# Kernel tuning notes

Hardware: AMD Instinct MI355X
Metric: run time of the kernel (lower is better)

Reference implementation:

```python
import jax, jax.numpy as jnp
import numpy as np

VOCAB = 50000
BATCH = 1024
SEQ = 120
NFEAT = 1
EMBED = 50
HIDDEN = 300
NCLASS = 5
FORGET_BIAS = 1.0  # tf.nn.rnn_cell.LSTMCell default


def setup_inputs() -> dict:
    key = jax.random.key(0)
    k1, k2, k3, k4 = jax.random.split(key, 4)
    input_ids = jax.random.randint(k1, (BATCH, SEQ, NFEAT), 0, VOCAB)
    embeddings = jax.random.normal(k2, (VOCAB, EMBED), jnp.float32)
    # LSTM kernel acts on concat([x, h]) -> 4*H gates (i, j, f, o order, TF convention)
    in_dim = NFEAT * EMBED + HIDDEN
    W_lstm = jax.random.normal(k3, (in_dim, 4 * HIDDEN), jnp.float32) * (1.0 / np.sqrt(in_dim))
    b_lstm = jnp.zeros((4 * HIDDEN,), jnp.float32)
    U = jax.random.normal(k4, (HIDDEN, NCLASS), jnp.float32) * (1.0 / np.sqrt(HIDDEN))
    b2 = jnp.zeros((NCLASS,), jnp.float32)
    return {"input_ids": input_ids, "embeddings": embeddings,
            "W_lstm": W_lstm, "b_lstm": b_lstm, "U": U, "b2": b2}


def reference(input_ids, embeddings, W_lstm, b_lstm, U, b2):
    B, T, F = input_ids.shape
    # embedding lookup + flatten feature dim: (B, T, F*E)
    x = embeddings[input_ids].reshape(B, T, -1)
    H = b_lstm.shape[0] // 4

    def cell(carry, x_t):
        c, h = carry
        z = jnp.concatenate([x_t, h], axis=-1) @ W_lstm + b_lstm  # (B, 4H)
        i, j, f, o = jnp.split(z, 4, axis=-1)  # TF LSTMCell gate order
        c_new = c * jax.nn.sigmoid(f + FORGET_BIAS) + jax.nn.sigmoid(i) * jnp.tanh(j)
        h_new = jnp.tanh(c_new) * jax.nn.sigmoid(o)
        return (c_new, h_new), h_new

    c0 = jnp.zeros((B, H), x.dtype)
    h0 = jnp.zeros((B, H), x.dtype)
    # scan over time; outputs are (T, B, H) which matches the module's final
    # transpose([1,0,2]) of the (B, T, C) preds.
    _, outs = jax.lax.scan(cell, (c0, h0), jnp.swapaxes(x, 0, 1))
    # dropout placeholder is 1.0 at inference -> identity
    preds = outs @ U + b2  # (T, B, n_classes)
    return preds
```

## Files before the change

kernel.cpp:

```cpp
#include <hip/hip_runtime.h>
#include <hip/hip_bf16.h>


#define NB 1024
#define NT 120
#define NE 50
#define NH 300
#define KX 64
#define KH 320
#define KT 384
#define HP 320
#define NGRP 8
#define NCOLB 19
#define ROLES 20
#define GRID 160
#define WCOL_STRIDE 784
#define HSLOTS 8

typedef __bf16 bf16_t;
typedef __bf16 bf16x8 __attribute__((ext_vector_type(8)));
typedef float f32x4 __attribute__((ext_vector_type(4)));

__device__ __forceinline__ float fsig(float x) {
    return __builtin_amdgcn_rcpf(1.0f + __expf(-x));
}
__device__ __forceinline__ float ftanh(float x) {
    return fmaf(2.0f, __builtin_amdgcn_rcpf(1.0f + __expf(-2.0f * x)), -1.0f);
}

__device__ __forceinline__ bf16x8 coh_load8(const bf16_t* p) {
    const unsigned long long* q = (const unsigned long long*)p;
    union { unsigned long long u[2]; bf16x8 v; } t;
    t.u[0] = __hip_atomic_load(q,     __ATOMIC_RELAXED, __HIP_MEMORY_SCOPE_AGENT);
    t.u[1] = __hip_atomic_load(q + 1, __ATOMIC_RELAXED, __HIP_MEMORY_SCOPE_AGENT);
    return t.v;
}
__device__ __forceinline__ void coh_store16(bf16_t* p, bf16_t h) {
    __hip_atomic_store((unsigned short*)p, __builtin_bit_cast(unsigned short, h),
                       __ATOMIC_RELAXED, __HIP_MEMORY_SCOPE_AGENT);
}
__device__ __forceinline__ unsigned coh_loadu(const unsigned* p) {
    return __hip_atomic_load(p, __ATOMIC_RELAXED, __HIP_MEMORY_SCOPE_AGENT);
}
__device__ __forceinline__ void cnt_bump(unsigned* p) {
    __hip_atomic_fetch_add(p, 1u, __ATOMIC_RELAXED, __HIP_MEMORY_SCOPE_AGENT);
}

__device__ __forceinline__ void inv_l1() {
    asm volatile("buffer_inv sc0\n\ts_waitcnt vmcnt(0)" ::: "memory");
}
__device__ __forceinline__ unsigned xcc_id() {
    unsigned x;
    asm volatile("s_getreg_b32 %0, hwreg(HW_REG_XCC_ID)" : "=s"(x));
    return x & 0xfu;
}

__global__ void prep_all(const int* __restrict__ ids, const float* __restrict__ emb,
                         const float* __restrict__ W,
                         bf16_t* __restrict__ WpT, uint4* __restrict__ zbase,
                         int nzero, bf16_t* __restrict__ Xp) {
    const long stride = (long)gridDim.x * 256;
    const long g0 = (long)blockIdx.x * 256 + threadIdx.x;

    for (long i = g0; i < nzero; i += stride)
        zbase[i] = make_uint4(0u, 0u, 0u, 0u);

    for (long gid = g0; gid < 4 * HP * KT; gid += stride) {
        int k = (int)(gid % KT);
        int col = (int)(gid / KT);
        int g = col / HP, hc = col % HP;
        int kp = -1;
        if (k < 50) kp = k;
        else if (k >= 64 && k < 364) kp = k - 14;
        float v = 0.0f;
        if (kp >= 0 && hc < NH) v = W[(long)kp * 1200 + g * NH + hc];
        WpT[gid] = (bf16_t)v;
    }

    for (long gid = g0; gid < (long)NB * NT * 4; gid += stride) {
        int s = (int)(gid & 3);
        long bt = gid >> 2;
        int b = (int)(bt / NT), t = (int)(bt % NT);
        int id = ids[bt];
        const float* er = emb + (long)id * NE;
        bf16_t* dst = Xp + ((long)t * NB + b) * KX + s * 16;
#pragma unroll
        for (int j = 0; j < 16; ++j) {
            int e = s * 16 + j;
            dst[j] = (bf16_t)((e < NE) ? er[e] : 0.0f);
        }
    }
}

__global__ void __launch_bounds__(512, 2) lstm_persist(
    const float* __restrict__ bl, const bf16_t* __restrict__ WpT,
    bf16_t* Hbase,
    const bf16_t* __restrict__ Xp,
    unsigned* gcnt, unsigned* pcnt, unsigned* xcdA,
    const float* __restrict__ U, const float* __restrict__ b2,
    float* __restrict__ out)
{
    __shared__ __align__(16) unsigned char smem[64 * WCOL_STRIDE];
    __shared__ int sLocalOK;
    const int blk = blockIdx.x;
    const int tid = threadIdx.x;
    const int g = blk & 7;
    const int c = blk >> 3;
    const int lane = tid & 63, wave = tid >> 6;

    if (tid == 0)
        __hip_atomic_store(xcdA + blk, xcc_id() + 1u,
                           __ATOMIC_RELAXED, __HIP_MEMORY_SCOPE_AGENT);
    if (wave == 0) {
        unsigned v = 1u;
        for (;;) {
            if (lane < ROLES)
                v = coh_loadu(xcdA + (lane * NGRP + g));
            if (__all(v != 0)) break;
            __builtin_amdgcn_s_sleep(1);
        }
        unsigned ref = __shfl(v, 0, 64);
        int ok = __all(lane >= ROLES || v == ref);
        if (lane == 0) sLocalOK = ok;
    }

    unsigned* gC = gcnt + (long)g * NT;
    unsigned* pC = pcnt + (long)g * NT;
    const size_t HSZ = (size_t)NB * KH;

    if (c < NCOLB) {
        for (int ch = tid; ch < 64 * 48; ch += 512) {
            int col = ch / 48, pq = ch % 48;
            int gt = col >> 4, mm = col & 15;
            int hc = c * 16 + mm;
            const uint4* src = (const uint4*)(WpT + (long)(gt * HP + hc) * KT) + pq;
            *(uint4*)(smem + col * WCOL_STRIDE + pq * 16) = *src;
        }

        const int m = lane & 15, quad = lane >> 4;
        const int rbase = g * 128 + wave * 16;
        const int rowA  = rbase + m;
        const int hcOut = c * 16 + m;
        const bool colOK = (hcOut < NH);

        float bias[4] = {0.f, 0.f, 0.f, 0.f};
        if (colOK) {
#pragma unroll
            for (int gt = 0; gt < 4; ++gt) bias[gt] = bl[gt * NH + hcOut];
        }
        float cst[4] = {0.f, 0.f, 0.f, 0.f};

        __syncthreads();
        const bool localOK = (sLocalOK != 0);

        bf16x8 Bh[8][4];
#pragma unroll
        for (int kk = 0; kk < 8; ++kk)
#pragma unroll
            for (int gt = 0; gt < 4; ++gt) {
                Bh[kk][gt] = *(const bf16x8*)(smem + (gt * 16 + m) * WCOL_STRIDE
                                              + ((kk + 2) * 4 + quad) * 16);
                asm volatile("" : "+v"(Bh[kk][gt]));
            }

        for (int t = 0; t < NT; ++t) {
            const bf16x8* xv = (const bf16x8*)(Xp + ((long)t * NB + rowA) * KX);
            bf16x8 ax[2];
#pragma unroll
            for (int kk = 0; kk < 2; ++kk) ax[kk] = xv[kk * 4 + quad];

            f32x4 acc[4];
#pragma unroll
            for (int gt = 0; gt < 4; ++gt)
                acc[gt] = (f32x4){bias[gt], bias[gt], bias[gt], bias[gt]};
#pragma unroll
            for (int kk = 0; kk < 2; ++kk) {
#pragma unroll
                for (int gt = 0; gt < 4; ++gt) {
                    bf16x8 b = *(const bf16x8*)(smem + (gt * 16 + m) * WCOL_STRIDE
                                                + (kk * 4 + quad) * 16);
                    acc[gt] = __builtin_amdgcn_mfma_f32_16x16x32_bf16(ax[kk], b, acc[gt], 0, 0, 0);
                }
            }

            if (t > 0) {
                if (wave == 0) {
                    unsigned* gcp = gC + (t - 1);
                    unsigned* pcp = pC + (t - HSLOTS);
                    const bool needP = (t >= HSLOTS);
                    for (;;) {
                        unsigned v = 19u;
                        if (lane == 0)               v = coh_loadu(gcp);
                        else if (lane == 1 && needP) v = 18u + coh_loadu(pcp);
                        if (__all(v >= 19u)) break;
                        __builtin_amdgcn_s_sleep(1);
                    }
                    if (localOK) inv_l1();
                }
            }
            __syncthreads();
            __builtin_amdgcn_sched_barrier(0);

            const bf16_t* Hr = Hbase + (size_t)((t + HSLOTS - 1) & (HSLOTS - 1)) * HSZ;
            bf16_t*       Hw = Hbase + (size_t)(t & (HSLOTS - 1)) * HSZ;

            const bf16_t* hp = Hr + (long)rowA * KH;
            bf16x8 ah[10];
            if (localOK) {
                const bf16x8* hv = (const bf16x8*)hp;
#pragma unroll
                for (int i = 0; i < 10; ++i) ah[i] = hv[i * 4 + quad];
            } else {
#pragma unroll
                for (int i = 0; i < 10; ++i) ah[i] = coh_load8(hp + (i * 4 + quad) * 8);
            }
            __builtin_amdgcn_sched_barrier(0);

#pragma unroll
            for (int kk = 2; kk < 10; ++kk) {
#pragma unroll
                for (int gt = 0; gt < 4; ++gt)
                    acc[gt] = __builtin_amdgcn_mfma_f32_16x16x32_bf16(
                        ah[kk - 2], Bh[kk - 2][gt], acc[gt], 0, 0, 0);
            }
#pragma unroll
            for (int kk = 10; kk < 12; ++kk) {
#pragma unroll
                for (int gt = 0; gt < 4; ++gt) {
                    bf16x8 b = *(const bf16x8*)(smem + (gt * 16 + m) * WCOL_STRIDE
                                                + (kk * 4 + quad) * 16);
                    acc[gt] = __builtin_amdgcn_mfma_f32_16x16x32_bf16(ah[kk - 2], b, acc[gt], 0, 0, 0);
                }
            }

#pragma unroll
            for (int r = 0; r < 4; ++r) {
                float zi = acc[0][r];
                float zj = acc[1][r];
                float zf = acc[2][r];
                float zo = acc[3][r];
                float cn = cst[r] * fsig(zf + 1.0f) + fsig(zi) * ftanh(zj);
                cst[r] = cn;
                float hn = ftanh(cn) * fsig(zo);
                if (colOK) {
                    bf16_t* dst = Hw + (long)(rbase + quad * 4 + r) * KH + hcOut;
                    if (localOK) *dst = (bf16_t)hn;
                    else coh_store16(dst, (bf16_t)hn);
                }
            }

            __syncthreads();
            if (tid == 0) cnt_bump(gC + t);
        }
    } else {
        bf16_t* UThi = (bf16_t*)smem;
        bf16_t* UTlo = (bf16_t*)(smem + 10240);
        for (int i = tid; i < 16 * 320; i += 512) {
            int n = i / 320, k = i % 320;
            float v = (n < 5 && k < NH) ? U[k * 5 + n] : 0.0f;
            bf16_t hi = (bf16_t)v;
            UThi[i] = hi;
            UTlo[i] = (bf16_t)(v - (float)hi);
        }
        const int m = lane & 15, quad = lane >> 4;
        const float b2v = (m < 5) ? b2[m] : 0.0f;
        __syncthreads();
        const bool localOK = (sLocalOK != 0);

        bf16x8 Bu[10][2];
#pragma unroll
        for (int kk = 0; kk < 10; ++kk) {
            Bu[kk][0] = *(const bf16x8*)(UThi + m * 320 + kk * 32 + quad * 8);
            asm volatile("" : "+v"(Bu[kk][0]));
            Bu[kk][1] = *(const bf16x8*)(UTlo + m * 320 + kk * 32 + quad * 8);
            asm volatile("" : "+v"(Bu[kk][1]));
        }
        const int row0 = g * 128 + wave * 16 + m;

        for (int t = 0; t < NT; ++t) {
            if (wave == 0) {
                unsigned* gcp = gC + t;
                for (;;) {
                    unsigned v = 19u;
                    if (lane == 0) v = coh_loadu(gcp);
                    if (__all(v >= 19u)) break;
                    __builtin_amdgcn_s_sleep(1);
                }
                if (localOK) inv_l1();
            }
            __syncthreads();
            __builtin_amdgcn_sched_barrier(0);

            const bf16_t* Hs = Hbase + (size_t)(t & (HSLOTS - 1)) * HSZ;
            const bf16_t* hp = Hs + (long)row0 * KH;
            bf16x8 ah[10];
            if (localOK) {
                const bf16x8* hv = (const bf16x8*)hp;
#pragma unroll
                for (int i = 0; i < 10; ++i) ah[i] = hv[i * 4 + quad];
            } else {
#pragma unroll
                for (int i = 0; i < 10; ++i) ah[i] = coh_load8(hp + (i * 4 + quad) * 8);
            }
            __builtin_amdgcn_sched_barrier(0);

            f32x4 acc = (f32x4){0.f, 0.f, 0.f, 0.f};
#pragma unroll
            for (int kk = 0; kk < 10; ++kk) {
                acc = __builtin_amdgcn_mfma_f32_16x16x32_bf16(ah[kk], Bu[kk][0], acc, 0, 0, 0);
                acc = __builtin_amdgcn_mfma_f32_16x16x32_bf16(ah[kk], Bu[kk][1], acc, 0, 0, 0);
            }

            if (m < 5) {
#pragma unroll
                for (int r = 0; r < 4; ++r) {
                    int row = g * 128 + wave * 16 + quad * 4 + r;
                    out[(long)t * (NB * 5) + row * 5 + m] = acc[r] + b2v;
                }
            }

            __syncthreads();
            if (tid == 0) cnt_bump(pC + t);
        }
    }
}

extern "C" void kernel_launch(void* const* d_in, const int* in_sizes, int n_in,
                              void* d_out, int out_size, void* d_ws, size_t ws_size,
                              hipStream_t stream) {
    const int* ids   = (const int*)d_in[0];
    const float* emb = (const float*)d_in[1];
    const float* W   = (const float*)d_in[2];
    const float* bl  = (const float*)d_in[3];
    const float* U   = (const float*)d_in[4];
    const float* b2  = (const float*)d_in[5];
    float* out = (float*)d_out;

    char* ws = (char*)d_ws;
    bf16_t*   WpT   = (bf16_t*)ws;
    bf16_t*   Hbase = (bf16_t*)(ws + 983040);
    unsigned* gcnt  = (unsigned*)(ws + 6225920);
    unsigned* pcnt  = (unsigned*)(ws + 6229760);
    unsigned* xcdA  = (unsigned*)(ws + 6233600);
    bf16_t*   Xp    = (bf16_t*)(ws + 6234240);

    prep_all<<<2048, 256, 0, stream>>>(ids, emb, W, WpT,
                                       (uint4*)(ws + 983040), 328200, Xp);

    void* kargs[] = { (void*)&bl, (void*)&WpT, (void*)&Hbase, (void*)&Xp,
                      (void*)&gcnt, (void*)&pcnt, (void*)&xcdA,
                      (void*)&U, (void*)&b2, (void*)&out };
    hipError_t err = hipLaunchCooperativeKernel((const void*)lstm_persist,
                                                dim3(GRID), dim3(512), kargs, 0, stream);
    if (err != hipSuccess) {
        lstm_persist<<<GRID, 512, 0, stream>>>(bl, WpT, Hbase, Xp,
                                               gcnt, pcnt, xcdA, U, b2, out);
    }
}
```

Baseline: 641.5 us.

## Halve waves per block and keep all LSTM weights in registers

Each block now runs 4 waves instead of 8, and each wave handles two 16-row tiles. Every weight fragment, including the input and tail K-slices, now sits in registers loaded straight from global memory, so the LDS staging and the per-step LDS weight reads are gone. The aim is to cut LDS traffic and synchronisation per step and to reuse each weight fragment across two row tiles. The cost is much higher register pressure per wave and fewer waves to hide the latency of the h loads and the MFMA chain.

```diff
diff --git a/kernel.cpp b/kernel.cpp
--- a/kernel.cpp
+++ b/kernel.cpp
@@ -14,7 +14,6 @@
 #define NCOLB 19
 #define ROLES 20
 #define GRID 160
-#define WCOL_STRIDE 784
 #define HSLOTS 8
 
 typedef __bf16 bf16_t;
@@ -92,7 +91,7 @@
     }
 }
 
-__global__ void __launch_bounds__(512, 2) lstm_persist(
+__global__ void __launch_bounds__(256, 1) lstm_persist(
     const float* __restrict__ bl, const bf16_t* __restrict__ WpT,
     bf16_t* Hbase,
     const bf16_t* __restrict__ Xp,
@@ -100,7 +99,7 @@
     const float* __restrict__ U, const float* __restrict__ b2,
     float* __restrict__ out)
 {
-    __shared__ __align__(16) unsigned char smem[64 * WCOL_STRIDE];
+    __shared__ __align__(16) unsigned char smem[20608];
     __shared__ int sLocalOK;
     const int blk = blockIdx.x;
     const int tid = threadIdx.x;
@@ -127,19 +126,12 @@
     unsigned* gC = gcnt + (long)g * NT;
     unsigned* pC = pcnt + (long)g * NT;
     const size_t HSZ = (size_t)NB * KH;
+    const int m = lane & 15, quad = lane >> 4;
 
     if (c < NCOLB) {
-        for (int ch = tid; ch < 64 * 48; ch += 512) {
-            int col = ch / 48, pq = ch % 48;
-            int gt = col >> 4, mm = col & 15;
-            int hc = c * 16 + mm;
-            const uint4* src = (const uint4*)(WpT + (long)(gt * HP + hc) * KT) + pq;
-            *(uint4*)(smem + col * WCOL_STRIDE + pq * 16) = *src;
-        }
-
-        const int m = lane & 15, quad = lane >> 4;
-        const int rbase = g * 128 + wave * 16;
-        const int rowA  = rbase + m;
+        const int rbase = g * 128 + wave * 32;
+        const int rowA0 = rbase + m;
+        const int rowA1 = rbase + 16 + m;
         const int hcOut = c * 16 + m;
         const bool colOK = (hcOut < NH);
 
@@ -148,38 +140,43 @@
 #pragma unroll
             for (int gt = 0; gt < 4; ++gt) bias[gt] = bl[gt * NH + hcOut];
         }
-        float cst[4] = {0.f, 0.f, 0.f, 0.f};
+        float cst[2][4] = {};
+
+        bf16x8 B[12][4];
+#pragma unroll
+        for (int kk = 0; kk < 12; ++kk)
+#pragma unroll
+            for (int gt = 0; gt < 4; ++gt) {
+                B[kk][gt] = *(const bf16x8*)(WpT + ((long)(gt * HP + hcOut) * KT)
+                                             + kk * 32 + quad * 8);
+                asm volatile("" : "+v"(B[kk][gt]));
+            }
 
         __syncthreads();
         const bool localOK = (sLocalOK != 0);
 
-        bf16x8 Bh[8][4];
-#pragma unroll
-        for (int kk = 0; kk < 8; ++kk)
-#pragma unroll
-            for (int gt = 0; gt < 4; ++gt) {
-                Bh[kk][gt] = *(const bf16x8*)(smem + (gt * 16 + m) * WCOL_STRIDE
-                                              + ((kk + 2) * 4 + quad) * 16);
-                asm volatile("" : "+v"(Bh[kk][gt]));
-            }
-
         for (int t = 0; t < NT; ++t) {
-            const bf16x8* xv = (const bf16x8*)(Xp + ((long)t * NB + rowA) * KX);
-            bf16x8 ax[2];
-#pragma unroll
-            for (int kk = 0; kk < 2; ++kk) ax[kk] = xv[kk * 4 + quad];
-
-            f32x4 acc[4];
-#pragma unroll
-            for (int gt = 0; gt < 4; ++gt)
-                acc[gt] = (f32x4){bias[gt], bias[gt], bias[gt], bias[gt]};
+            const bf16x8* xv0 = (const bf16x8*)(Xp + ((long)t * NB + rowA0) * KX);
+            const bf16x8* xv1 = (const bf16x8*)(Xp + ((long)t * NB + rowA1) * KX);
+            bf16x8 ax0[2], ax1[2];
 #pragma unroll
             for (int kk = 0; kk < 2; ++kk) {
+                ax0[kk] = xv0[kk * 4 + quad];
+                ax1[kk] = xv1[kk * 4 + quad];
+            }
+
+            f32x4 acc[2][4];
+#pragma unroll
+            for (int rt = 0; rt < 2; ++rt)
+#pragma unroll
+                for (int gt = 0; gt < 4; ++gt)
+                    acc[rt][gt] = (f32x4){bias[gt], bias[gt], bias[gt], bias[gt]};
+#pragma unroll
+            for (int kk = 0; kk < 2; ++kk) {
 #pragma unroll
                 for (int gt = 0; gt < 4; ++gt) {
-                    bf16x8 b = *(const bf16x8*)(smem + (gt * 16 + m) * WCOL_STRIDE
-                                                + (kk * 4 + quad) * 16);
-                    acc[gt] = __builtin_amdgcn_mfma_f32_16x16x32_bf16(ax[kk], b, acc[gt], 0, 0, 0);
+                    acc[0][gt] = __builtin_amdgcn_mfma_f32_16x16x32_bf16(ax0[kk], B[kk][gt], acc[0][gt], 0, 0, 0);
+                    acc[1][gt] = __builtin_amdgcn_mfma_f32_16x16x32_bf16(ax1[kk], B[kk][gt], acc[1][gt], 0, 0, 0);
                 }
             }
 
@@ -204,48 +201,51 @@
             const bf16_t* Hr = Hbase + (size_t)((t + HSLOTS - 1) & (HSLOTS - 1)) * HSZ;
             bf16_t*       Hw = Hbase + (size_t)(t & (HSLOTS - 1)) * HSZ;
 
-            const bf16_t* hp = Hr + (long)rowA * KH;
-            bf16x8 ah[10];
+            const bf16_t* h0p = Hr + (long)rowA0 * KH;
+            const bf16_t* h1p = Hr + (long)rowA1 * KH;
+            bf16x8 ah0[10], ah1[10];
             if (localOK) {
-                const bf16x8* hv = (const bf16x8*)hp;
-#pragma unroll
-                for (int i = 0; i < 10; ++i) ah[i] = hv[i * 4 + quad];
+                const bf16x8* hv0 = (const bf16x8*)h0p;
+                const bf16x8* hv1 = (const bf16x8*)h1p;
+#pragma unroll
+                for (int i = 0; i < 10; ++i) {
+                    ah0[i] = hv0[i * 4 + quad];
+                    ah1[i] = hv1[i * 4 + quad];
+                }
             } else {
 #pragma unroll
-                for (int i = 0; i < 10; ++i) ah[i] = coh_load8(hp + (i * 4 + quad) * 8);
+                for (int i = 0; i < 10; ++i) {
+                    ah0[i] = coh_load8(h0p + (i * 4 + quad) * 8);
+                    ah1[i] = coh_load8(h1p + (i * 4 + quad) * 8);
+                }
             }
             __builtin_amdgcn_sched_barrier(0);
 
 #pragma unroll
-            for (int kk = 2; kk < 10; ++kk) {
-#pragma unroll
-                for (int gt = 0; gt < 4; ++gt)
-                    acc[gt] = __builtin_amdgcn_mfma_f32_16x16x32_bf16(
-                        ah[kk - 2], Bh[kk - 2][gt], acc[gt], 0, 0, 0);
-            }
-#pragma unroll
-            for (int kk = 10; kk < 12; ++kk) {
+            for (int kk = 2; kk < 12; ++kk) {
 #pragma unroll
                 for (int gt = 0; gt < 4; ++gt) {
-                    bf16x8 b = *(const bf16x8*)(smem + (gt * 16 + m) * WCOL_STRIDE
-                                                + (kk * 4 + quad) * 16);
-                    acc[gt] = __builtin_amdgcn_mfma_f32_16x16x32_bf16(ah[kk - 2], b, acc[gt], 0, 0, 0);
-                }
-            }
-
-#pragma unroll
-            for (int r = 0; r < 4; ++r) {
-                float zi = acc[0][r];
-                float zj = acc[1][r];
-                float zf = acc[2][r];
-                float zo = acc[3][r];
-                float cn = cst[r] * fsig(zf + 1.0f) + fsig(zi) * ftanh(zj);
-                cst[r] = cn;
-                float hn = ftanh(cn) * fsig(zo);
-                if (colOK) {
-                    bf16_t* dst = Hw + (long)(rbase + quad * 4 + r) * KH + hcOut;
-                    if (localOK) *dst = (bf16_t)hn;
-                    else coh_store16(dst, (bf16_t)hn);
+                    acc[0][gt] = __builtin_amdgcn_mfma_f32_16x16x32_bf16(ah0[kk - 2], B[kk][gt], acc[0][gt], 0, 0, 0);
+                    acc[1][gt] = __builtin_amdgcn_mfma_f32_16x16x32_bf16(ah1[kk - 2], B[kk][gt], acc[1][gt], 0, 0, 0);
+                }
+            }
+
+#pragma unroll
+            for (int rt = 0; rt < 2; ++rt) {
+#pragma unroll
+                for (int r = 0; r < 4; ++r) {
+                    float zi = acc[rt][0][r];
+                    float zj = acc[rt][1][r];
+                    float zf = acc[rt][2][r];
+                    float zo = acc[rt][3][r];
+                    float cn = cst[rt][r] * fsig(zf + 1.0f) + fsig(zi) * ftanh(zj);
+                    cst[rt][r] = cn;
+                    float hn = ftanh(cn) * fsig(zo);
+                    if (colOK) {
+                        bf16_t* dst = Hw + (long)(rbase + rt * 16 + quad * 4 + r) * KH + hcOut;
+                        if (localOK) *dst = (bf16_t)hn;
+                        else coh_store16(dst, (bf16_t)hn);
+                    }
                 }
             }
 
@@ -255,14 +255,13 @@
     } else {
         bf16_t* UThi = (bf16_t*)smem;
         bf16_t* UTlo = (bf16_t*)(smem + 10240);
-        for (int i = tid; i < 16 * 320; i += 512) {
+        for (int i = tid; i < 16 * 320; i += 256) {
             int n = i / 320, k = i % 320;
             float v = (n < 5 && k < NH) ? U[k * 5 + n] : 0.0f;
             bf16_t hi = (bf16_t)v;
             UThi[i] = hi;
             UTlo[i] = (bf16_t)(v - (float)hi);
         }
-        const int m = lane & 15, quad = lane >> 4;
         const float b2v = (m < 5) ? b2[m] : 0.0f;
         __syncthreads();
         const bool localOK = (sLocalOK != 0);
@@ -275,7 +274,9 @@
             Bu[kk][1] = *(const bf16x8*)(UTlo + m * 320 + kk * 32 + quad * 8);
             asm volatile("" : "+v"(Bu[kk][1]));
         }
-        const int row0 = g * 128 + wave * 16 + m;
+        const int rbase = g * 128 + wave * 32;
+        const int row0 = rbase + m;
+        const int row1 = rbase + 16 + m;
 
         for (int t = 0; t < NT; ++t) {
             if (wave == 0) {
@@ -292,30 +293,43 @@
             __builtin_amdgcn_sched_barrier(0);
 
             const bf16_t* Hs = Hbase + (size_t)(t & (HSLOTS - 1)) * HSZ;
-            const bf16_t* hp = Hs + (long)row0 * KH;
-            bf16x8 ah[10];
+            const bf16_t* h0p = Hs + (long)row0 * KH;
+            const bf16_t* h1p = Hs + (long)row1 * KH;
+            bf16x8 ah0[10], ah1[10];
             if (localOK) {
-                const bf16x8* hv = (const bf16x8*)hp;
-#pragma unroll
-                for (int i = 0; i < 10; ++i) ah[i] = hv[i * 4 + quad];
+                const bf16x8* hv0 = (const bf16x8*)h0p;
+                const bf16x8* hv1 = (const bf16x8*)h1p;
+#pragma unroll
+                for (int i = 0; i < 10; ++i) {
+                    ah0[i] = hv0[i * 4 + quad];
+                    ah1[i] = hv1[i * 4 + quad];
+                }
             } else {
 #pragma unroll
-                for (int i = 0; i < 10; ++i) ah[i] = coh_load8(hp + (i * 4 + quad) * 8);
+                for (int i = 0; i < 10; ++i) {
+                    ah0[i] = coh_load8(h0p + (i * 4 + quad) * 8);
+                    ah1[i] = coh_load8(h1p + (i * 4 + quad) * 8);
+                }
             }
             __builtin_amdgcn_sched_barrier(0);
 
-            f32x4 acc = (f32x4){0.f, 0.f, 0.f, 0.f};
+            f32x4 acc0 = (f32x4){0.f, 0.f, 0.f, 0.f};
+            f32x4 acc1 = (f32x4){0.f, 0.f, 0.f, 0.f};
 #pragma unroll
             for (int kk = 0; kk < 10; ++kk) {
-                acc = __builtin_amdgcn_mfma_f32_16x16x32_bf16(ah[kk], Bu[kk][0], acc, 0, 0, 0);
-                acc = __builtin_amdgcn_mfma_f32_16x16x32_bf16(ah[kk], Bu[kk][1], acc, 0, 0, 0);
+                acc0 = __builtin_amdgcn_mfma_f32_16x16x32_bf16(ah0[kk], Bu[kk][0], acc0, 0, 0, 0);
+                acc0 = __builtin_amdgcn_mfma_f32_16x16x32_bf16(ah0[kk], Bu[kk][1], acc0, 0, 0, 0);
+                acc1 = __builtin_amdgcn_mfma_f32_16x16x32_bf16(ah1[kk], Bu[kk][0], acc1, 0, 0, 0);
+                acc1 = __builtin_amdgcn_mfma_f32_16x16x32_bf16(ah1[kk], Bu[kk][1], acc1, 0, 0, 0);
             }
 
             if (m < 5) {
 #pragma unroll
                 for (int r = 0; r < 4; ++r) {
-                    int row = g * 128 + wave * 16 + quad * 4 + r;
-                    out[(long)t * (NB * 5) + row * 5 + m] = acc[r] + b2v;
+                    int ro0 = rbase + quad * 4 + r;
+                    int ro1 = rbase + 16 + quad * 4 + r;
+                    out[(long)t * (NB * 5) + ro0 * 5 + m] = acc0[r] + b2v;
+                    out[(long)t * (NB * 5) + ro1 * 5 + m] = acc1[r] + b2v;
                 }
             }
 
@@ -351,9 +365,9 @@
                       (void*)&gcnt, (void*)&pcnt, (void*)&xcdA,
                       (void*)&U, (void*)&b2, (void*)&out };
     hipError_t err = hipLaunchCooperativeKernel((const void*)lstm_persist,
-                                                dim3(GRID), dim3(512), kargs, 0, stream);
+                                                dim3(GRID), dim3(256), kargs, 0, stream);
     if (err != hipSuccess) {
-        lstm_persist<<<GRID, 512, 0, stream>>>(bl, WpT, Hbase, Xp,
+        lstm_persist<<<GRID, 256, 0, stream>>>(bl, WpT, Hbase, Xp,
                                                gcnt, pcnt, xcdA, U, b2, out);
     }
 }
```

Result: slower. 710.5 us (+10.8%).
